# Kernel optimization log

Hardware: AMD Instinct MI355X
Metric: run time of the kernel (lower is better)

## Reference

```python
import jax, jax.numpy as jnp
import numpy as np

N_CUST, N_PROD, N_EDGES, EMBED_DIM, HIDDEN = 100000, 100000, 1000000, 64, 64


def setup_inputs() -> dict:
    key = jax.random.key(0)
    ks = jax.random.split(key, 8)
    D = EMBED_DIM
    return {
        "h_customer": jax.random.normal(ks[0], (N_CUST, D), dtype=jnp.float32),
        "h_product": jax.random.normal(ks[1], (N_PROD, D), dtype=jnp.float32),
        "src_idx": jax.random.randint(ks[2], (N_EDGES,), 0, N_CUST),
        "dst_idx": jax.random.randint(ks[3], (N_EDGES,), 0, N_PROD),
        "W1": jax.random.normal(ks[4], (2 * D + 1, HIDDEN), dtype=jnp.float32) * 0.05,
        "b1": jnp.zeros((HIDDEN,), dtype=jnp.float32),
        "W2": jax.random.normal(ks[5], (HIDDEN, 1), dtype=jnp.float32) * 0.05,
        "b2": jnp.zeros((1,), dtype=jnp.float32),
    }


def reference(h_customer, h_product, src_idx, dst_idx, W1, b1, W2, b2):
    # Per-edge gather of head/tail node embeddings: [E, D]
    heads = h_customer[src_idx]
    tails = h_product[dst_idx]

    # F.normalize(p=2, dim=-1), torch eps = 1e-12
    hn = heads / jnp.maximum(jnp.linalg.norm(heads, axis=-1, keepdims=True), 1e-12)
    tn = tails / jnp.maximum(jnp.linalg.norm(tails, axis=-1, keepdims=True), 1e-12)

    # cosine_similarity of already-normalized vectors, torch eps = 1e-8
    denom = jnp.maximum(
        jnp.linalg.norm(hn, axis=-1) * jnp.linalg.norm(tn, axis=-1), 1e-8
    )
    cos = jnp.sum(hn * tn, axis=-1) / denom  # [E]

    # concat(raw heads, raw tails, cosine) -> [E, 2D+1]
    cat = jnp.concatenate([heads, tails, cos[:, None]], axis=1)

    # small prediction MLP -> sigmoid ratings, [E, 1]
    x = jax.nn.relu(cat @ W1 + b1)
    ratings = jax.nn.sigmoid(x @ W2 + b2)
    return ratings
```

## Files before the change

### kernel.cpp

```cpp
#include <hip/hip_runtime.h>
#include <math.h>


typedef __attribute__((ext_vector_type(8))) short bf16x8;
typedef __attribute__((ext_vector_type(4))) float f32x4;
typedef __attribute__((ext_vector_type(2))) float float2_t;
typedef __attribute__((ext_vector_type(8))) unsigned short ushort8_t;
typedef __attribute__((ext_vector_type(4))) float float4_t;
typedef __attribute__((ext_vector_type(4))) unsigned int uint4_t;
typedef __attribute__((ext_vector_type(2))) unsigned int uint2_t;

#define T_STRIDE 72
#define P_STRIDE 72

__device__ __forceinline__ float bf2f(unsigned short u) {
    return __uint_as_float(((unsigned int)u) << 16);
}
__device__ __forceinline__ unsigned short f2bf(float f) {
    unsigned int x = __float_as_uint(f);
    return (unsigned short)((x + 0x7fffu + ((x >> 16) & 1u)) >> 16);
}

__global__ __launch_bounds__(256) void prep_w1(
    const float* __restrict__ W1, unsigned short* __restrict__ frag)
{
    int idx = blockIdx.x * 256 + threadIdx.x;
    if (idx >= 2 * 4 * 2 * 64 * 8) return;
    int j    = idx & 7;
    int lane = (idx >> 3) & 63;
    int ks   = (idx >> 9) & 1;
    int nt   = (idx >> 10) & 3;
    int half = (idx >> 12) & 1;
    int k   = ks * 32 + (lane >> 4) * 8 + j;
    int col = nt * 16 + (lane & 15);
    frag[idx] = f2bf(W1[(half * 64 + k) * 64 + col]);
}

__global__ __launch_bounds__(256) void node_fused(
    const float* __restrict__ hc, const float* __restrict__ hp,
    const unsigned short* __restrict__ w1frag, const float* __restrict__ b1,
    unsigned char* __restrict__ recC, unsigned char* __restrict__ recP,
    int nC, int nP, int blocksC)
{
    __shared__ unsigned short tileA[64 * T_STRIDE];
    __shared__ unsigned short tile2[64 * P_STRIDE];
    __shared__ unsigned char  recs[64 * 128];

    int b = blockIdx.x;
    const float* h; unsigned char* rec; int n, half;
    if (b < blocksC) { h = hc; rec = recC; n = nC; half = 0; }
    else { b -= blocksC; h = hp; rec = recP; n = nP; half = 1; }

    int node0 = b * 64;
    int nloc  = min(64, n - node0);
    int t     = threadIdx.x;
    int nl    = t >> 2, q = t & 3;
    int wave  = t >> 6, lane = t & 63;
    int m = lane & 15, quad = lane >> 4;

    if (nl < nloc) {
        const float* srcp = h + (long)(node0 + nl) * 64 + q * 16;
        float4_t v[4];
#pragma unroll
        for (int i = 0; i < 4; i++)
            v[i] = *reinterpret_cast<const float4_t*>(srcp + i * 4);

        float ss = 0.f;
#pragma unroll
        for (int i = 0; i < 4; i++)
#pragma unroll
            for (int j = 0; j < 4; j++) ss += v[i][j] * v[i][j];
        ss += __shfl_xor(ss, 1);
        ss += __shfl_xor(ss, 2);
        float inv = 1.f / fmaxf(sqrtf(ss), 1e-12f);

        ushort8_t u[2];
#pragma unroll
        for (int i = 0; i < 16; i++) u[i >> 3][i & 7] = f2bf(v[i >> 2][i & 3]);
        *reinterpret_cast<ushort8_t*>(&tileA[nl * T_STRIDE + q * 16])     = u[0];
        *reinterpret_cast<ushort8_t*>(&tileA[nl * T_STRIDE + q * 16 + 8]) = u[1];

        uint4_t u8;
#pragma unroll
        for (int i = 0; i < 4; i++) {
            unsigned int d = __builtin_amdgcn_cvt_pk_fp8_f32(
                v[i][0] * inv, v[i][1] * inv, 0, false);
            d = __builtin_amdgcn_cvt_pk_fp8_f32(
                v[i][2] * inv, v[i][3] * inv, d, true);
            u8[i] = d;
        }
        *reinterpret_cast<uint4_t*>(&recs[nl * 128 + q * 16]) = u8;
    }
    __syncthreads();

    if (wave * 16 < nloc) {
        bf16x8 a[2];
#pragma unroll
        for (int ks = 0; ks < 2; ks++)
            a[ks] = *reinterpret_cast<const bf16x8*>(
                &tileA[(wave * 16 + m) * T_STRIDE + ks * 32 + quad * 8]);

        f32x4 acc[4];
#pragma unroll
        for (int nt = 0; nt < 4; nt++) acc[nt] = (f32x4){0.f, 0.f, 0.f, 0.f};
#pragma unroll
        for (int nt = 0; nt < 4; nt++)
#pragma unroll
            for (int ks = 0; ks < 2; ks++) {
                bf16x8 bf = *reinterpret_cast<const bf16x8*>(
                    &w1frag[(((half * 4 + nt) * 2 + ks) * 64 + lane) * 8]);
                acc[nt] = __builtin_amdgcn_mfma_f32_16x16x32_bf16(
                    a[ks], bf, acc[nt], 0, 0, 0);
            }
        if (half == 0) {
#pragma unroll
            for (int nt = 0; nt < 4; nt++) {
                float bb = b1[nt * 16 + m];
#pragma unroll
                for (int r = 0; r < 4; r++) acc[nt][r] += bb;
            }
        }
#pragma unroll
        for (int nt = 0; nt < 4; nt++)
#pragma unroll
            for (int r = 0; r < 4; r++)
                tile2[(wave * 16 + quad * 4 + r) * P_STRIDE + nt * 16 + m]
                    = f2bf(acc[nt][r]);
    }
    __syncthreads();

    if (nl < nloc) {
        ushort8_t p0 = *reinterpret_cast<ushort8_t*>(&tile2[nl * P_STRIDE + q * 16]);
        ushort8_t p1 = *reinterpret_cast<ushort8_t*>(&tile2[nl * P_STRIDE + q * 16 + 8]);
        float v[16];
#pragma unroll
        for (int i = 0; i < 8; i++) { v[i] = bf2f(p0[i]); v[i + 8] = bf2f(p1[i]); }
        uint4_t u;
#pragma unroll
        for (int i = 0; i < 4; i++) {
            unsigned int d = __builtin_amdgcn_cvt_pk_fp8_f32(
                v[i * 4 + 0], v[i * 4 + 1], 0, false);
            d = __builtin_amdgcn_cvt_pk_fp8_f32(
                v[i * 4 + 2], v[i * 4 + 3], d, true);
            u[i] = d;
        }
        *reinterpret_cast<uint4_t*>(&recs[nl * 128 + 64 + q * 16]) = u;
    }
    __syncthreads();

    if (t * 32 < nloc * 128) {
        uint4_t r0 = *reinterpret_cast<uint4_t*>(&recs[t * 32]);
        uint4_t r1 = *reinterpret_cast<uint4_t*>(&recs[t * 32 + 16]);
        unsigned char* dstp = rec + (long)node0 * 128 + t * 32;
        *reinterpret_cast<uint4_t*>(dstp)      = r0;
        *reinterpret_cast<uint4_t*>(dstp + 16) = r1;
    }
}

__global__ __launch_bounds__(256) void edge_mlp(
    const unsigned char* __restrict__ recC, const unsigned char* __restrict__ recP,
    const int* __restrict__ src, const int* __restrict__ dst,
    const float* __restrict__ W1, const float* __restrict__ W2,
    const float* __restrict__ b2, float* __restrict__ out, int nE)
{
    int lane = threadIdx.x & 63;
    int sub  = lane >> 2;
    int g    = lane & 3;
    int d0   = g * 16;
    int wid  = (blockIdx.x * 256 + threadIdx.x) >> 6;

    int e0 = wid * 32 + sub;
    int e1 = e0 + 16;
    bool v0 = e0 < nE, v1 = e1 < nE;
    int s0 = v0 ? src[e0] : 0, t0 = v0 ? dst[e0] : 0;
    int s1 = v1 ? src[e1] : 0, t1 = v1 ? dst[e1] : 0;

    const unsigned char* rs0 = recC + (long)s0 * 128;
    const unsigned char* rt0 = recP + (long)t0 * 128;
    const unsigned char* rs1 = recC + (long)s1 * 128;
    const unsigned char* rt1 = recP + (long)t1 * 128;
    uint4_t hs0 = *reinterpret_cast<const uint4_t*>(rs0 + d0);
    uint4_t ht0 = *reinterpret_cast<const uint4_t*>(rt0 + d0);
    uint4_t ps0 = *reinterpret_cast<const uint4_t*>(rs0 + 64 + d0);
    uint4_t pt0 = *reinterpret_cast<const uint4_t*>(rt0 + 64 + d0);
    uint4_t hs1 = *reinterpret_cast<const uint4_t*>(rs1 + d0);
    uint4_t ht1 = *reinterpret_cast<const uint4_t*>(rt1 + d0);
    uint4_t ps1 = *reinterpret_cast<const uint4_t*>(rs1 + 64 + d0);
    uint4_t pt1 = *reinterpret_cast<const uint4_t*>(rt1 + 64 + d0);

    float4_t w1v[4], w2v[4];
#pragma unroll
    for (int i = 0; i < 4; i++) {
        w1v[i] = *reinterpret_cast<const float4_t*>(W1 + 128 * 64 + d0 + i * 4);
        w2v[i] = *reinterpret_cast<const float4_t*>(W2 + d0 + i * 4);
    }
    float b2v = b2[0];

#pragma unroll
    for (int batch = 0; batch < 2; batch++) {
        uint4_t hs = batch ? hs1 : hs0;
        uint4_t ht = batch ? ht1 : ht0;
        uint4_t ps = batch ? ps1 : ps0;
        uint4_t pt = batch ? pt1 : pt0;

        float dot = 0.f;
#pragma unroll
        for (int w = 0; w < 4; w++) {
            float2_t alo = __builtin_amdgcn_cvt_pk_f32_fp8((int)hs[w], false);
            float2_t ahi = __builtin_amdgcn_cvt_pk_f32_fp8((int)hs[w], true);
            float2_t blo = __builtin_amdgcn_cvt_pk_f32_fp8((int)ht[w], false);
            float2_t bhi = __builtin_amdgcn_cvt_pk_f32_fp8((int)ht[w], true);
            dot += alo[0] * blo[0] + alo[1] * blo[1] + ahi[0] * bhi[0] + ahi[1] * bhi[1];
        }
        dot += __shfl_xor(dot, 1);
        dot += __shfl_xor(dot, 2);
        float cosv = dot;

        float p = 0.f;
#pragma unroll
        for (int w = 0; w < 4; w++) {
            float2_t clo = __builtin_amdgcn_cvt_pk_f32_fp8((int)ps[w], false);
            float2_t chi = __builtin_amdgcn_cvt_pk_f32_fp8((int)ps[w], true);
            float2_t dlo = __builtin_amdgcn_cvt_pk_f32_fp8((int)pt[w], false);
            float2_t dhi = __builtin_amdgcn_cvt_pk_f32_fp8((int)pt[w], true);
            float pcv[4] = {clo[0], clo[1], chi[0], chi[1]};
            float ppv[4] = {dlo[0], dlo[1], dhi[0], dhi[1]};
#pragma unroll
            for (int j = 0; j < 4; j++) {
                float x = pcv[j] + ppv[j] + cosv * w1v[w][j];
                x = fmaxf(x, 0.f);
                p += x * w2v[w][j];
            }
        }
        p += __shfl_xor(p, 1);
        p += __shfl_xor(p, 2);

        int e = batch ? e1 : e0;
        bool valid = batch ? v1 : v0;
        if (valid && g == 0)
            out[e] = 1.f / (1.f + expf(-(p + b2v)));
    }
}

extern "C" void kernel_launch(void* const* d_in, const int* in_sizes, int n_in,
                              void* d_out, int out_size, void* d_ws, size_t ws_size,
                              hipStream_t stream) {
    const float* h_c = (const float*)d_in[0];
    const float* h_p = (const float*)d_in[1];
    const int*   src = (const int*)d_in[2];
    const int*   dst = (const int*)d_in[3];
    const float* W1  = (const float*)d_in[4];
    const float* b1  = (const float*)d_in[5];
    const float* W2  = (const float*)d_in[6];
    const float* b2  = (const float*)d_in[7];
    float* out = (float*)d_out;

    int nC = in_sizes[0] / 64;
    int nP = in_sizes[1] / 64;
    int nE = in_sizes[2];

    char* ws = (char*)d_ws;
    size_t off = 0;
    auto carve = [&](size_t bytes) {
        void* p = ws + off;
        off = (off + bytes + 255) & ~(size_t)255;
        return p;
    };
    unsigned char* recC = (unsigned char*)carve((size_t)nC * 128);
    unsigned char* recP = (unsigned char*)carve((size_t)nP * 128);
    unsigned short* w1f = (unsigned short*)carve((size_t)16384 * 2);

    prep_w1<<<64, 256, 0, stream>>>(W1, w1f);

    int blocksC = (nC + 63) / 64, blocksP = (nP + 63) / 64;
    node_fused<<<blocksC + blocksP, 256, 0, stream>>>(
        h_c, h_p, w1f, b1, recC, recP, nC, nP, blocksC);

    edge_mlp<<<(nE + 127) / 128, 256, 0, stream>>>(
        recC, recP, src, dst, W1, W2, b2, out, nE);
}
```

Measured before the change: 140.2 us.

## Remap edge gather to 8 lanes per edge and batch six edges per wave

The edge kernel now gives each edge 8 lanes, each loading 16 contiguous bytes of the 128-byte node record. Previously each edge used 4 lanes issuing two loads apiece. Each wave now handles 48 edges in six batches, with all index and record loads issued up front so more gathers are in flight. Half the lanes compute the cosine partial and the other half the projected-hidden partial, joined through an extra shuffle. This costs more registers (launch bounds hint 4 blocks) and leaves half the lanes idle in the MLP step.

```diff
diff --git a/kernel.cpp b/kernel.cpp
--- a/kernel.cpp
+++ b/kernel.cpp
@@ -157,88 +157,89 @@
     }
 }
 
-__global__ __launch_bounds__(256) void edge_mlp(
+#define NB 6
+__global__ __launch_bounds__(256, 4) void edge_mlp(
     const unsigned char* __restrict__ recC, const unsigned char* __restrict__ recP,
     const int* __restrict__ src, const int* __restrict__ dst,
     const float* __restrict__ W1, const float* __restrict__ W2,
     const float* __restrict__ b2, float* __restrict__ out, int nE)
 {
     int lane = threadIdx.x & 63;
-    int sub  = lane >> 2;
-    int g    = lane & 3;
-    int d0   = g * 16;
+    int sub  = lane >> 3;
+    int g    = lane & 7;
     int wid  = (blockIdx.x * 256 + threadIdx.x) >> 6;
-
-    int e0 = wid * 32 + sub;
-    int e1 = e0 + 16;
-    bool v0 = e0 < nE, v1 = e1 < nE;
-    int s0 = v0 ? src[e0] : 0, t0 = v0 ? dst[e0] : 0;
-    int s1 = v1 ? src[e1] : 0, t1 = v1 ? dst[e1] : 0;
-
-    const unsigned char* rs0 = recC + (long)s0 * 128;
-    const unsigned char* rt0 = recP + (long)t0 * 128;
-    const unsigned char* rs1 = recC + (long)s1 * 128;
-    const unsigned char* rt1 = recP + (long)t1 * 128;
-    uint4_t hs0 = *reinterpret_cast<const uint4_t*>(rs0 + d0);
-    uint4_t ht0 = *reinterpret_cast<const uint4_t*>(rt0 + d0);
-    uint4_t ps0 = *reinterpret_cast<const uint4_t*>(rs0 + 64 + d0);
-    uint4_t pt0 = *reinterpret_cast<const uint4_t*>(rt0 + 64 + d0);
-    uint4_t hs1 = *reinterpret_cast<const uint4_t*>(rs1 + d0);
-    uint4_t ht1 = *reinterpret_cast<const uint4_t*>(rt1 + d0);
-    uint4_t ps1 = *reinterpret_cast<const uint4_t*>(rs1 + 64 + d0);
-    uint4_t pt1 = *reinterpret_cast<const uint4_t*>(rt1 + 64 + d0);
-
+    int base = wid * (NB * 8);
+
+    int ed[NB]; int sI[NB], tI[NB]; bool vd[NB];
+#pragma unroll
+    for (int b = 0; b < NB; b++) {
+        ed[b] = base + b * 8 + sub;
+        vd[b] = ed[b] < nE;
+        sI[b] = vd[b] ? src[ed[b]] : 0;
+        tI[b] = vd[b] ? dst[ed[b]] : 0;
+    }
+
+    uint4_t cs[NB], ct[NB];
+#pragma unroll
+    for (int b = 0; b < NB; b++) {
+        cs[b] = *reinterpret_cast<const uint4_t*>(
+            recC + (long)sI[b] * 128 + g * 16);
+        ct[b] = *reinterpret_cast<const uint4_t*>(
+            recP + (long)tI[b] * 128 + g * 16);
+    }
+
+    int d0p = (g & 3) * 16;
     float4_t w1v[4], w2v[4];
 #pragma unroll
     for (int i = 0; i < 4; i++) {
-        w1v[i] = *reinterpret_cast<const float4_t*>(W1 + 128 * 64 + d0 + i * 4);
-        w2v[i] = *reinterpret_cast<const float4_t*>(W2 + d0 + i * 4);
+        w1v[i] = *reinterpret_cast<const float4_t*>(W1 + 128 * 64 + d0p + i * 4);
+        w2v[i] = *reinterpret_cast<const float4_t*>(W2 + d0p + i * 4);
     }
     float b2v = b2[0];
 
 #pragma unroll
-    for (int batch = 0; batch < 2; batch++) {
-        uint4_t hs = batch ? hs1 : hs0;
-        uint4_t ht = batch ? ht1 : ht0;
-        uint4_t ps = batch ? ps1 : ps0;
-        uint4_t pt = batch ? pt1 : pt0;
+    for (int b = 0; b < NB; b++) {
+        uint4_t a = cs[b];
+        uint4_t c = ct[b];
 
         float dot = 0.f;
 #pragma unroll
         for (int w = 0; w < 4; w++) {
-            float2_t alo = __builtin_amdgcn_cvt_pk_f32_fp8((int)hs[w], false);
-            float2_t ahi = __builtin_amdgcn_cvt_pk_f32_fp8((int)hs[w], true);
-            float2_t blo = __builtin_amdgcn_cvt_pk_f32_fp8((int)ht[w], false);
-            float2_t bhi = __builtin_amdgcn_cvt_pk_f32_fp8((int)ht[w], true);
+            float2_t alo = __builtin_amdgcn_cvt_pk_f32_fp8((int)a[w], false);
+            float2_t ahi = __builtin_amdgcn_cvt_pk_f32_fp8((int)a[w], true);
+            float2_t blo = __builtin_amdgcn_cvt_pk_f32_fp8((int)c[w], false);
+            float2_t bhi = __builtin_amdgcn_cvt_pk_f32_fp8((int)c[w], true);
             dot += alo[0] * blo[0] + alo[1] * blo[1] + ahi[0] * bhi[0] + ahi[1] * bhi[1];
         }
         dot += __shfl_xor(dot, 1);
         dot += __shfl_xor(dot, 2);
-        float cosv = dot;
+        float ov   = __shfl_xor(dot, 4);
+        float cosv = (g & 4) ? ov : dot;
 
         float p = 0.f;
-#pragma unroll
-        for (int w = 0; w < 4; w++) {
-            float2_t clo = __builtin_amdgcn_cvt_pk_f32_fp8((int)ps[w], false);
-            float2_t chi = __builtin_amdgcn_cvt_pk_f32_fp8((int)ps[w], true);
-            float2_t dlo = __builtin_amdgcn_cvt_pk_f32_fp8((int)pt[w], false);
-            float2_t dhi = __builtin_amdgcn_cvt_pk_f32_fp8((int)pt[w], true);
-            float pcv[4] = {clo[0], clo[1], chi[0], chi[1]};
-            float ppv[4] = {dlo[0], dlo[1], dhi[0], dhi[1]};
-#pragma unroll
-            for (int j = 0; j < 4; j++) {
-                float x = pcv[j] + ppv[j] + cosv * w1v[w][j];
-                x = fmaxf(x, 0.f);
-                p += x * w2v[w][j];
+        if (g & 4) {
+#pragma unroll
+            for (int w = 0; w < 4; w++) {
+                float2_t clo = __builtin_amdgcn_cvt_pk_f32_fp8((int)a[w], false);
+                float2_t chi = __builtin_amdgcn_cvt_pk_f32_fp8((int)a[w], true);
+                float2_t dlo = __builtin_amdgcn_cvt_pk_f32_fp8((int)c[w], false);
+                float2_t dhi = __builtin_amdgcn_cvt_pk_f32_fp8((int)c[w], true);
+                float pcv[4] = {clo[0], clo[1], chi[0], chi[1]};
+                float ppv[4] = {dlo[0], dlo[1], dhi[0], dhi[1]};
+#pragma unroll
+                for (int j = 0; j < 4; j++) {
+                    float x = pcv[j] + ppv[j] + cosv * w1v[w][j];
+                    x = fmaxf(x, 0.f);
+                    p += x * w2v[w][j];
+                }
             }
         }
         p += __shfl_xor(p, 1);
         p += __shfl_xor(p, 2);
-
-        int e = batch ? e1 : e0;
-        bool valid = batch ? v1 : v0;
-        if (valid && g == 0)
-            out[e] = 1.f / (1.f + expf(-(p + b2v)));
+        p += __shfl_xor(p, 4);
+
+        if (vd[b] && g == 0)
+            out[ed[b]] = 1.f / (1.f + expf(-(p + b2v)));
     }
 }
 
@@ -276,6 +277,6 @@
     node_fused<<<blocksC + blocksP, 256, 0, stream>>>(
         h_c, h_p, w1f, b1, recC, recP, nC, nP, blocksC);
 
-    edge_mlp<<<(nE + 127) / 128, 256, 0, stream>>>(
+    edge_mlp<<<(nE + 191) / 192, 256, 0, stream>>>(
         recC, recP, src, dst, W1, W2, b2, out, nE);
 }
```

Measured after the change: 156.5 us. +11.7%, slower.
